# Kernel optimization log

Measured on AMD Instinct MI355X. Metric: run time of the kernel, lower is better.

The kernel has to match this reference:

```python
import jax, jax.numpy as jnp
import numpy as np

N = 100000   # nodes
E = 1600000  # edges (avg degree 16)
G = 512      # graphs in batch
IN = 96      # in_channels
H = 128      # hidden_channels
C = 100      # num_classes
ED = 8       # edge_dim
L = 4        # num_layers
EPS_LN = 1e-5


def setup_inputs() -> dict:
    key = jax.random.key(0)
    ks = jax.random.split(key, 24)
    s = 0.05
    d = {
        "x": jax.random.normal(ks[0], (N, IN), jnp.float32),
        "edge_index": jax.random.randint(ks[1], (2, E), 0, N, jnp.int32),
        "batch": jnp.sort(jax.random.randint(ks[2], (N,), 0, G, jnp.int32)),
        "edge_attr": jax.random.normal(ks[3], (E, ED), jnp.float32),
        # edge encoder MLP: Linear(ED,H) -> ReLU -> Linear(H,1)
        "ee_W1": jax.random.normal(ks[4], (ED, H), jnp.float32) * s,
        "ee_b1": jnp.zeros((H,), jnp.float32),
        "ee_W2": jax.random.normal(ks[5], (H, 1), jnp.float32) * s,
        "ee_b2": jnp.zeros((1,), jnp.float32),
        # GCNConv weights (PyG: lin without bias, bias added after aggregation)
        "W0": jax.random.normal(ks[6], (IN, H), jnp.float32) * s,
        "cb0": jnp.zeros((H,), jnp.float32),
        "W1": jax.random.normal(ks[7], (H, H), jnp.float32) * s,
        "cb1": jnp.zeros((H,), jnp.float32),
        "W2": jax.random.normal(ks[8], (H, H), jnp.float32) * s,
        "cb2": jnp.zeros((H,), jnp.float32),
        "W3": jax.random.normal(ks[9], (H, H), jnp.float32) * s,
        "cb3": jnp.zeros((H,), jnp.float32),
        # LayerNorm params
        "g0": jnp.ones((H,), jnp.float32), "be0": jnp.zeros((H,), jnp.float32),
        "g1": jnp.ones((H,), jnp.float32), "be1": jnp.zeros((H,), jnp.float32),
        "g2": jnp.ones((H,), jnp.float32), "be2": jnp.zeros((H,), jnp.float32),
        "g3": jnp.ones((H,), jnp.float32), "be3": jnp.zeros((H,), jnp.float32),
        # residual projection for layer 0 only (IN != H)
        "res_W": jax.random.normal(ks[10], (IN, H), jnp.float32) * s,
        "res_b": jnp.zeros((H,), jnp.float32),
        # head: Linear(2H,H) -> ReLU -> Linear(H,C)
        "hW1": jax.random.normal(ks[11], (2 * H, H), jnp.float32) * s,
        "hb1": jnp.zeros((H,), jnp.float32),
        "hW2": jax.random.normal(ks[12], (H, C), jnp.float32) * s,
        "hb2": jnp.zeros((C,), jnp.float32),
    }
    return d


def _layer_norm(h, g, b):
    mu = jnp.mean(h, axis=-1, keepdims=True)
    var = jnp.mean(jnp.square(h - mu), axis=-1, keepdims=True)
    return g * (h - mu) / jnp.sqrt(var + EPS_LN) + b


def reference(x, edge_index, batch, edge_attr,
              ee_W1, ee_b1, ee_W2, ee_b2,
              W0, cb0, W1, cb1, W2, cb2, W3, cb3,
              g0, be0, g1, be1, g2, be2, g3, be3,
              res_W, res_b, hW1, hb1, hW2, hb2):
    row, col = edge_index[0], edge_index[1]

    # edge weight = softplus(MLP(edge_attr)) + 1e-4  -> [E]
    eh = jax.nn.relu(edge_attr @ ee_W1 + ee_b1)
    ew = jax.nn.softplus((eh @ ee_W2 + ee_b2)[:, 0]) + 1e-4

    # add self loops with weight 1 (PyG GCNConv default)
    loops = jnp.arange(N, dtype=row.dtype)
    row_sl = jnp.concatenate([row, loops])
    col_sl = jnp.concatenate([col, loops])
    ew_sl = jnp.concatenate([ew, jnp.ones((N,), ew.dtype)])

    # symmetric normalization: D^-1/2 A D^-1/2 (deg over target index)
    deg = jax.ops.segment_sum(ew_sl, col_sl, num_segments=N)
    dis = jnp.where(deg > 0, jax.lax.rsqrt(deg), 0.0)
    norm = dis[row_sl] * ew_sl * dis[col_sl]  # [E+N]

    def conv(h, W, b):
        hw = h @ W                                   # [N,H]
        msg = hw[row_sl] * norm[:, None]             # [E+N,H]
        return jax.ops.segment_sum(msg, col_sl, num_segments=N) + b

    Ws = [W0, W1, W2, W3]
    cbs = [cb0, cb1, cb2, cb3]
    gs = [g0, g1, g2, g3]
    bes = [be0, be1, be2, be3]

    hidden = []
    cur = x
    for i in range(L):
        h = conv(cur, Ws[i], cbs[i])
        h = _layer_norm(h, gs[i], bes[i])
        res = cur @ res_W + res_b if i == 0 else cur
        h = jax.nn.relu(h + res)
        # dropout: eval mode -> identity
        hidden.append(h)
        cur = h
    xm = jnp.mean(jnp.stack(hidden, axis=0), axis=0)  # [N,H]

    # meanmax pooling over graphs
    counts = jax.ops.segment_sum(jnp.ones((N,), xm.dtype), batch, num_segments=G)
    gmean = jax.ops.segment_sum(xm, batch, num_segments=G) / jnp.maximum(counts, 1.0)[:, None]
    gmax = jax.ops.segment_max(xm, batch, num_segments=G)
    gmax = jnp.where(jnp.isfinite(gmax), gmax, 0.0)
    g = jnp.concatenate([gmean, gmax], axis=-1)       # [G,2H]

    # head (dropout identity in eval)
    return jax.nn.relu(g @ hW1 + hb1) @ hW2 + hb2     # [G,C]
```

## Files before the change

kernel.cpp:

```cpp
#include <hip/hip_runtime.h>
#include <hip/hip_fp16.h>
#include <math.h>

#define NN 100000
#define EE 1600000
#define GB 512
#define INC 96
#define HH 128
#define CC 100
#define MAXD 64

typedef __bf16 bf16x8 __attribute__((ext_vector_type(8)));
typedef _Float16 f16x8 __attribute__((ext_vector_type(8)));
typedef float f32x4 __attribute__((ext_vector_type(4)));

__device__ __forceinline__ float unpack_w_f32(unsigned v) {
    return __half2float(__ushort_as_half((unsigned short)(v & 0x7FFFu)));
}
__device__ __forceinline__ __half2 unpack_w_h2(unsigned v) {
    __half h = __ushort_as_half((unsigned short)(v & 0x7FFFu));
    return __halves2half2(h, h);
}

__global__ __launch_bounds__(256) void k_cast(const float* __restrict__ src, __half* __restrict__ dst, int n4) {
    int i = blockIdx.x * 256 + threadIdx.x;
    if (i >= n4) return;
    float4 v = *(const float4*)&src[(size_t)i * 4];
    __half2 a = __floats2half2_rn(v.x, v.y);
    __half2 b = __floats2half2_rn(v.z, v.w);
    *(__half2*)&dst[(size_t)i * 4]     = a;
    *(__half2*)&dst[(size_t)i * 4 + 2] = b;
}

__global__ __launch_bounds__(256) void k_castT(const float* __restrict__ W, __half* __restrict__ Wt, int K) {
    int idx = blockIdx.x * 256 + threadIdx.x;
    if (idx >= K * 128) return;
    int k = idx >> 7, n = idx & 127;
    Wt[(size_t)n * K + k] = __float2half(W[idx]);
}

__global__ __launch_bounds__(512) void k_prep_w1(const float* __restrict__ W1, __bf16* __restrict__ w1f) {
    int tid = threadIdx.x;
    int t = tid >> 6, lane = tid & 63;
    int ln15 = lane & 15, quad = lane >> 4;
    bf16x8 v = {};
    if (quad == 0) {
#pragma unroll
        for (int j = 0; j < 8; ++j) v[j] = (__bf16)W1[j * 128 + t * 16 + ln15];
    }
    *(bf16x8*)&w1f[(size_t)(t * 64 + lane) * 8] = v;
}

__global__ __launch_bounds__(256) void k_edge_mlp_mfma(
    const float* __restrict__ ea,
    const __bf16* __restrict__ w1f, const float* __restrict__ b1,
    const float* __restrict__ W2, const float* __restrict__ b2,
    const int* __restrict__ ei, int* __restrict__ cnt, unsigned* __restrict__ epack)
{
    __shared__ float sDot[128];
    int tid = threadIdx.x, wva = tid >> 6, lane = tid & 63;
    int ln15 = lane & 15, quad = lane >> 4;
    int ebase = blockIdx.x * 128 + wva * 32;

    bf16x8 bfr[8];
#pragma unroll
    for (int t = 0; t < 8; ++t) bfr[t] = *(const bf16x8*)&w1f[(size_t)(t * 64 + lane) * 8];

    bf16x8 a0 = {}, a1 = {};
    if (quad == 0) {
        const float* p0 = &ea[(size_t)(ebase + ln15) * 8];
        float4 u0 = *(const float4*)p0, u1 = *(const float4*)(p0 + 4);
        a0[0] = (__bf16)u0.x; a0[1] = (__bf16)u0.y; a0[2] = (__bf16)u0.z; a0[3] = (__bf16)u0.w;
        a0[4] = (__bf16)u1.x; a0[5] = (__bf16)u1.y; a0[6] = (__bf16)u1.z; a0[7] = (__bf16)u1.w;
        const float* p1 = &ea[(size_t)(ebase + 16 + ln15) * 8];
        float4 w0 = *(const float4*)p1, w1v = *(const float4*)(p1 + 4);
        a1[0] = (__bf16)w0.x; a1[1] = (__bf16)w0.y; a1[2] = (__bf16)w0.z; a1[3] = (__bf16)w0.w;
        a1[4] = (__bf16)w1v.x; a1[5] = (__bf16)w1v.y; a1[6] = (__bf16)w1v.z; a1[7] = (__bf16)w1v.w;
    }

    f32x4 d0 = {0.f, 0.f, 0.f, 0.f}, d1 = {0.f, 0.f, 0.f, 0.f};
#pragma unroll
    for (int t = 0; t < 8; ++t) {
        f32x4 z = {0.f, 0.f, 0.f, 0.f};
        f32x4 c0 = __builtin_amdgcn_mfma_f32_16x16x32_bf16(a0, bfr[t], z, 0, 0, 0);
        f32x4 c1 = __builtin_amdgcn_mfma_f32_16x16x32_bf16(a1, bfr[t], z, 0, 0, 0);
        int col = t * 16 + ln15;
        float b1v = b1[col], w2v = W2[col];
#pragma unroll
        for (int r = 0; r < 4; ++r) {
            float v0 = fmaxf(c0[r] + b1v, 0.0f);
            float v1 = fmaxf(c1[r] + b1v, 0.0f);
            d0[r] = fmaf(v0, w2v, d0[r]);
            d1[r] = fmaf(v1, w2v, d1[r]);
        }
    }
#pragma unroll
    for (int o = 1; o < 16; o <<= 1) {
#pragma unroll
        for (int r = 0; r < 4; ++r) {
            d0[r] += __shfl_xor(d0[r], o, 64);
            d1[r] += __shfl_xor(d1[r], o, 64);
        }
    }
    if (ln15 == 0) {
#pragma unroll
        for (int r = 0; r < 4; ++r) {
            sDot[wva * 32 + quad * 4 + r]      = d0[r];
            sDot[wva * 32 + 16 + quad * 4 + r] = d1[r];
        }
    }
    __syncthreads();
    if (tid < 128) {
        int e = blockIdx.x * 128 + tid;
        float x = sDot[tid] + b2[0];
        float sp = (x > 20.0f) ? x : log1pf(expf(x));
        float wgt = sp + 1e-4f;
        int r = ei[e], c = ei[EE + e];
        int rank = atomicAdd(&cnt[c], 1);
        if (rank < MAXD) {
            unsigned hb = (unsigned)__half_as_ushort(__float2half(wgt)) & 0x7FFFu;
            epack[(size_t)c * MAXD + rank] = ((unsigned)r << 15) | hb;
        }
    }
}

__global__ __launch_bounds__(256) void k_degk(int* __restrict__ cnt, const unsigned* __restrict__ epack,
                                              float* __restrict__ dis, int n) {
    int i = blockIdx.x * 256 + threadIdx.x;
    if (i >= n) return;
    int c = cnt[i]; c = c < MAXD ? c : MAXD;
    cnt[i] = c;
    const unsigned* base = &epack[(size_t)i * MAXD];
    float d = 1.0f;
    for (int k = 0; k < c; ++k) d += unpack_w_f32(base[k]);
    dis[i] = rsqrtf(d);
}

__global__ __launch_bounds__(256) void k_norm(const int* __restrict__ cnt, const float* __restrict__ dis,
                                              unsigned* __restrict__ epack, int n) {
    int wv = threadIdx.x >> 6, lane = threadIdx.x & 63;
    int i = blockIdx.x * 4 + wv;
    if (i >= n) return;
    float dc = dis[i];
    if (lane < cnt[i]) {
        unsigned v = epack[(size_t)i * MAXD + lane];
        float wn = dis[v >> 15] * unpack_w_f32(v) * dc;
        unsigned hb = (unsigned)__half_as_ushort(__float2half(wn)) & 0x7FFFu;
        epack[(size_t)i * MAXD + lane] = (v & 0xFFFF8000u) | hb;
    }
}

__global__ __launch_bounds__(256) void k_gemm_f16(
    const __half* __restrict__ A, const __half* __restrict__ Bt,
    const float* __restrict__ bias, __half* __restrict__ C, int M, int K)
{
    int tid = threadIdx.x;
    int wv = tid >> 6, lane = tid & 63;
    int ln15 = lane & 15, quad = lane >> 4;
    int m0 = blockIdx.x * 64;
    int n0 = wv * 32;
    f32x4 acc[4][2];
#pragma unroll
    for (int mt = 0; mt < 4; ++mt)
#pragma unroll
        for (int nt = 0; nt < 2; ++nt) acc[mt][nt] = (f32x4){0.f, 0.f, 0.f, 0.f};

    int rowm[4];
#pragma unroll
    for (int mt = 0; mt < 4; ++mt) {
        int r = m0 + mt * 16 + ln15;
        rowm[mt] = r < M ? r : M - 1;
    }
    for (int kc = 0; kc < K; kc += 32) {
        f16x8 af[4], bfr[2];
#pragma unroll
        for (int mt = 0; mt < 4; ++mt)
            af[mt] = *(const f16x8*)&A[(size_t)rowm[mt] * K + kc + quad * 8];
#pragma unroll
        for (int nt = 0; nt < 2; ++nt)
            bfr[nt] = *(const f16x8*)&Bt[(size_t)(n0 + nt * 16 + ln15) * K + kc + quad * 8];
#pragma unroll
        for (int mt = 0; mt < 4; ++mt)
#pragma unroll
            for (int nt = 0; nt < 2; ++nt)
                acc[mt][nt] = __builtin_amdgcn_mfma_f32_16x16x32_f16(af[mt], bfr[nt], acc[mt][nt], 0, 0, 0);
    }
#pragma unroll
    for (int nt = 0; nt < 2; ++nt) {
        int col = n0 + nt * 16 + ln15;
        float bv = bias ? bias[col] : 0.0f;
#pragma unroll
        for (int mt = 0; mt < 4; ++mt) {
#pragma unroll
            for (int r = 0; r < 4; ++r) {
                int row = m0 + mt * 16 + quad * 4 + r;
                if (row < M) C[(size_t)row * 128 + col] = __float2half(acc[mt][nt][r] + bv);
            }
        }
    }
}

__global__ __launch_bounds__(256) void k_agg_ln(
    const __half* __restrict__ hw, const float* __restrict__ dis,
    const int* __restrict__ cnt, const unsigned* __restrict__ epack,
    const float* __restrict__ cb, const float* __restrict__ gam,
    const float* __restrict__ bet, const __half* __restrict__ res,
    __half* __restrict__ out, int n)
{
    int wv = threadIdx.x >> 6;
    int lane = threadIdx.x & 63;
    int i = blockIdx.x * 4 + wv;
    if (i >= n) return;
    float di = dis[i];
    float sn = di * di;
    __half2 own = *(const __half2*)&hw[(size_t)i * HH + lane * 2];
    __half hsn = __float2half(sn);
    __half2 acc = __hmul2(own, __halves2half2(hsn, hsn));
    int cn = cnt[i];
    const unsigned* ebase = &epack[(size_t)i * MAXD];
    int k = 0;
    for (; k + 8 <= cn; k += 8) {
        uint4 q0 = *(const uint4*)&ebase[k];
        uint4 q1 = *(const uint4*)&ebase[k + 4];
        __half2 v0 = *(const __half2*)&hw[(size_t)(q0.x >> 15) * HH + lane * 2];
        __half2 v1 = *(const __half2*)&hw[(size_t)(q0.y >> 15) * HH + lane * 2];
        __half2 v2 = *(const __half2*)&hw[(size_t)(q0.z >> 15) * HH + lane * 2];
        __half2 v3 = *(const __half2*)&hw[(size_t)(q0.w >> 15) * HH + lane * 2];
        __half2 v4 = *(const __half2*)&hw[(size_t)(q1.x >> 15) * HH + lane * 2];
        __half2 v5 = *(const __half2*)&hw[(size_t)(q1.y >> 15) * HH + lane * 2];
        __half2 v6 = *(const __half2*)&hw[(size_t)(q1.z >> 15) * HH + lane * 2];
        __half2 v7 = *(const __half2*)&hw[(size_t)(q1.w >> 15) * HH + lane * 2];
        acc = __hfma2(v0, unpack_w_h2(q0.x), acc);
        acc = __hfma2(v1, unpack_w_h2(q0.y), acc);
        acc = __hfma2(v2, unpack_w_h2(q0.z), acc);
        acc = __hfma2(v3, unpack_w_h2(q0.w), acc);
        acc = __hfma2(v4, unpack_w_h2(q1.x), acc);
        acc = __hfma2(v5, unpack_w_h2(q1.y), acc);
        acc = __hfma2(v6, unpack_w_h2(q1.z), acc);
        acc = __hfma2(v7, unpack_w_h2(q1.w), acc);
    }
    for (; k < cn; ++k) {
        unsigned e = ebase[k];
        __half2 v = *(const __half2*)&hw[(size_t)(e >> 15) * HH + lane * 2];
        acc = __hfma2(v, unpack_w_h2(e), acc);
    }
    float2 af = __half22float2(acc);
    float2 cbv = *(const float2*)&cb[lane * 2];
    af.x += cbv.x; af.y += cbv.y;
    float s1 = af.x + af.y;
    float s2 = af.x * af.x + af.y * af.y;
#pragma unroll
    for (int o = 32; o > 0; o >>= 1) {
        s1 += __shfl_xor(s1, o, 64);
        s2 += __shfl_xor(s2, o, 64);
    }
    float mean = s1 * (1.0f / HH);
    float var = fmaxf(s2 * (1.0f / HH) - mean * mean, 0.0f);
    float rstd = rsqrtf(var + 1e-5f);
    float2 gv = *(const float2*)&gam[lane * 2];
    float2 bv = *(const float2*)&bet[lane * 2];
    float2 rv = __half22float2(*(const __half2*)&res[(size_t)i * HH + lane * 2]);
    float hx = fmaxf(fmaf(gv.x, (af.x - mean) * rstd, bv.x) + rv.x, 0.0f);
    float hy = fmaxf(fmaf(gv.y, (af.y - mean) * rstd, bv.y) + rv.y, 0.0f);
    *(__half2*)&out[(size_t)i * HH + lane * 2] = __floats2half2_rn(hx, hy);
}

__global__ __launch_bounds__(128) void k_pool(
    const __half* __restrict__ l0, const __half* __restrict__ l1,
    const __half* __restrict__ l2, const __half* __restrict__ l3,
    const int* __restrict__ batch, float* __restrict__ gbuf, int n)
{
    int g = blockIdx.x, t = threadIdx.x;
    int lo = 0, hi = n;
    while (lo < hi) { int m = (lo + hi) >> 1; if (batch[m] < g) lo = m + 1; else hi = m; }
    int start = lo;
    lo = start; hi = n;
    while (lo < hi) { int m = (lo + hi) >> 1; if (batch[m] < g + 1) lo = m + 1; else hi = m; }
    int end = lo;
    float sum = 0.0f, mx = -INFINITY;
    for (int nd = start; nd < end; ++nd) {
        size_t off = (size_t)nd * HH + t;
        float v = (__half2float(l0[off]) + __half2float(l1[off]) +
                   __half2float(l2[off]) + __half2float(l3[off])) * 0.25f;
        sum += v;
        mx = fmaxf(mx, v);
    }
    int cntg = end - start;
    float mean = sum / fmaxf((float)cntg, 1.0f);
    gbuf[(size_t)g * 256 + t] = mean;
    gbuf[(size_t)g * 256 + 128 + t] = (cntg > 0) ? mx : 0.0f;
}

__global__ __launch_bounds__(128) void k_head(const float* __restrict__ gbuf,
                                              const float* __restrict__ hW1, const float* __restrict__ hb1,
                                              const float* __restrict__ hW2, const float* __restrict__ hb2,
                                              float* __restrict__ out) {
    __shared__ __align__(16) float sg[256];
    __shared__ __align__(16) float sh[128];
    int g = blockIdx.x, t = threadIdx.x;
    sg[t] = gbuf[(size_t)g * 256 + t];
    sg[t + 128] = gbuf[(size_t)g * 256 + 128 + t];
    __syncthreads();
    float h = hb1[t];
    for (int k = 0; k < 256; ++k) h = fmaf(sg[k], hW1[(size_t)k * 128 + t], h);
    sh[t] = fmaxf(h, 0.0f);
    __syncthreads();
    if (t < 100) {
        float o = hb2[t];
        for (int k = 0; k < 128; ++k) o = fmaf(sh[k], hW2[(size_t)k * 100 + t], o);
        out[(size_t)g * 100 + t] = o;
    }
}

extern "C" void kernel_launch(void* const* d_in, const int* in_sizes, int n_in,
                              void* d_out, int out_size, void* d_ws, size_t ws_size,
                              hipStream_t stream) {
    const float* x     = (const float*)d_in[0];
    const int*   ei    = (const int*)d_in[1];
    const int*   batch = (const int*)d_in[2];
    const float* ea    = (const float*)d_in[3];
    const float* eeW1  = (const float*)d_in[4];
    const float* eeb1  = (const float*)d_in[5];
    const float* eeW2  = (const float*)d_in[6];
    const float* eeb2  = (const float*)d_in[7];
    const float* W[4]  = {(const float*)d_in[8], (const float*)d_in[10], (const float*)d_in[12], (const float*)d_in[14]};
    const float* cb[4] = {(const float*)d_in[9], (const float*)d_in[11], (const float*)d_in[13], (const float*)d_in[15]};
    const float* gm[4] = {(const float*)d_in[16], (const float*)d_in[18], (const float*)d_in[20], (const float*)d_in[22]};
    const float* be[4] = {(const float*)d_in[17], (const float*)d_in[19], (const float*)d_in[21], (const float*)d_in[23]};
    const float* resW  = (const float*)d_in[24];
    const float* resb  = (const float*)d_in[25];
    const float* hW1   = (const float*)d_in[26];
    const float* hb1   = (const float*)d_in[27];
    const float* hW2   = (const float*)d_in[28];
    const float* hb2   = (const float*)d_in[29];
    float* out = (float*)d_out;

    char* w = (char*)d_ws;
    auto alloc = [&](size_t bytes) { void* p = w; w += (bytes + 255) & ~(size_t)255; return p; };
    float*    dis    = (float*)   alloc((size_t)NN * 4);
    int*      cnt    = (int*)     alloc((size_t)NN * 4);
    unsigned* epack  = (unsigned*)alloc((size_t)NN * MAXD * 4);
    __half*   xb     = (__half*)  alloc((size_t)NN * INC * 2);
    __half*   hw     = (__half*)  alloc((size_t)NN * HH * 2);
    __half*   lout[4];
    for (int i = 0; i < 4; ++i) lout[i] = (__half*)alloc((size_t)NN * HH * 2);
    float*    gbuf   = (float*)   alloc((size_t)GB * 256 * 4);
    __half*   wt0    = (__half*)  alloc((size_t)INC * HH * 2);
    __half*   wtR    = (__half*)  alloc((size_t)INC * HH * 2);
    __half*   wt1    = (__half*)  alloc((size_t)HH * HH * 2);
    __half*   wt2    = (__half*)  alloc((size_t)HH * HH * 2);
    __half*   wt3    = (__half*)  alloc((size_t)HH * HH * 2);
    __bf16*   w1f    = (__bf16*)  alloc((size_t)8 * 64 * 8 * 2);
    __half*   wtc[4] = {wt0, wt1, wt2, wt3};
    __half*   res0   = lout[1];

    int nblkN = (NN + 255) / 256;
    int nblkEdge = EE / 128;
    int nblkGemm = (NN + 63) / 64;
    int nblkCast = (NN * INC / 4 + 255) / 256;
    int nblkT96 = (INC * 128 + 255) / 256;
    int nblkT128 = (HH * 128 + 255) / 256;

    hipMemsetAsync(cnt, 0, (size_t)NN * 4, stream);
    k_cast<<<nblkCast, 256, 0, stream>>>(x, xb, NN * INC / 4);
    k_castT<<<nblkT96, 256, 0, stream>>>(W[0], wt0, INC);
    k_castT<<<nblkT96, 256, 0, stream>>>(resW, wtR, INC);
    k_castT<<<nblkT128, 256, 0, stream>>>(W[1], wt1, HH);
    k_castT<<<nblkT128, 256, 0, stream>>>(W[2], wt2, HH);
    k_castT<<<nblkT128, 256, 0, stream>>>(W[3], wt3, HH);
    k_prep_w1<<<1, 512, 0, stream>>>(eeW1, w1f);
    k_edge_mlp_mfma<<<nblkEdge, 256, 0, stream>>>(ea, w1f, eeb1, eeW2, eeb2, ei, cnt, epack);
    k_degk<<<nblkN, 256, 0, stream>>>(cnt, epack, dis, NN);
    k_norm<<<(NN + 3) / 4, 256, 0, stream>>>(cnt, dis, epack, NN);

    k_gemm_f16<<<nblkGemm, 256, 0, stream>>>(xb, wt0, nullptr, hw, NN, INC);
    k_gemm_f16<<<nblkGemm, 256, 0, stream>>>(xb, wtR, resb, res0, NN, INC);
    k_agg_ln<<<(NN + 3) / 4, 256, 0, stream>>>(hw, dis, cnt, epack,
                                               cb[0], gm[0], be[0], res0, lout[0], NN);
    for (int l = 1; l < 4; ++l) {
        k_gemm_f16<<<nblkGemm, 256, 0, stream>>>(lout[l - 1], wtc[l], nullptr, hw, NN, HH);
        k_agg_ln<<<(NN + 3) / 4, 256, 0, stream>>>(hw, dis, cnt, epack,
                                                   cb[l], gm[l], be[l], lout[l - 1], lout[l], NN);
    }

    k_pool<<<GB, 128, 0, stream>>>(lout[0], lout[1], lout[2], lout[3], batch, gbuf, NN);
    k_head<<<GB, 128, 0, stream>>>(gbuf, hW1, hb1, hW2, hb2, out);
}
```

Before: 854.3 us.

## Build CSR adjacency via two-pass bucketed scatter instead of global atomics

The edge MLP now only writes per-edge weights. A new split kernel bins edges by destination bucket of 512 nodes using shared-memory histograms and one global atomic per bucket per block. A build kernel then fills each node's packed adjacency list and degree using shared-memory atomics, which replaces the scattered global atomics and the separate degree kernel. The five weight transpose casts are merged into one launch. The cost is an extra edge-weight array and a bucket staging buffer with a fixed capacity per bucket, so edges past that capacity would be silently dropped.

After: 838.0 us. Within noise of the previous version (-1.9%).

```diff
diff --git a/kernel.cpp b/kernel.cpp
--- a/kernel.cpp
+++ b/kernel.cpp
@@ -9,6 +9,10 @@
 #define HH 128
 #define CC 100
 #define MAXD 64
+#define BUCKB 9
+#define NBUK 196
+#define CAPB 10240
+#define EB 4096
 
 typedef __bf16 bf16x8 __attribute__((ext_vector_type(8)));
 typedef _Float16 f16x8 __attribute__((ext_vector_type(8)));
@@ -32,11 +36,23 @@
     *(__half2*)&dst[(size_t)i * 4 + 2] = b;
 }
 
-__global__ __launch_bounds__(256) void k_castT(const float* __restrict__ W, __half* __restrict__ Wt, int K) {
+__global__ __launch_bounds__(256) void k_prep_weights(
+    const float* __restrict__ W0, const float* __restrict__ resW,
+    const float* __restrict__ W1m, const float* __restrict__ W2m, const float* __restrict__ W3m,
+    __half* __restrict__ wt0, __half* __restrict__ wtR,
+    __half* __restrict__ wt1, __half* __restrict__ wt2, __half* __restrict__ wt3)
+{
     int idx = blockIdx.x * 256 + threadIdx.x;
-    if (idx >= K * 128) return;
-    int k = idx >> 7, n = idx & 127;
-    Wt[(size_t)n * K + k] = __float2half(W[idx]);
+    const float* src; __half* dst; int K, base;
+    if (idx < 12288)      { src = W0;   dst = wt0; K = 96;  base = 0; }
+    else if (idx < 24576) { src = resW; dst = wtR; K = 96;  base = 12288; }
+    else if (idx < 40960) { src = W1m;  dst = wt1; K = 128; base = 24576; }
+    else if (idx < 57344) { src = W2m;  dst = wt2; K = 128; base = 40960; }
+    else if (idx < 73728) { src = W3m;  dst = wt3; K = 128; base = 57344; }
+    else return;
+    int l = idx - base;
+    int k = l >> 7, n = l & 127;
+    dst[(size_t)n * K + k] = __float2half(src[l]);
 }
 
 __global__ __launch_bounds__(512) void k_prep_w1(const float* __restrict__ W1, __bf16* __restrict__ w1f) {
@@ -55,7 +71,7 @@
     const float* __restrict__ ea,
     const __bf16* __restrict__ w1f, const float* __restrict__ b1,
     const float* __restrict__ W2, const float* __restrict__ b2,
-    const int* __restrict__ ei, int* __restrict__ cnt, unsigned* __restrict__ epack)
+    float* __restrict__ ew)
 {
     __shared__ float sDot[128];
     int tid = threadIdx.x, wva = tid >> 6, lane = tid & 63;
@@ -114,26 +130,71 @@
         int e = blockIdx.x * 128 + tid;
         float x = sDot[tid] + b2[0];
         float sp = (x > 20.0f) ? x : log1pf(expf(x));
-        float wgt = sp + 1e-4f;
-        int r = ei[e], c = ei[EE + e];
-        int rank = atomicAdd(&cnt[c], 1);
-        if (rank < MAXD) {
-            unsigned hb = (unsigned)__half_as_ushort(__float2half(wgt)) & 0x7FFFu;
-            epack[(size_t)c * MAXD + rank] = ((unsigned)r << 15) | hb;
-        }
-    }
-}
-
-__global__ __launch_bounds__(256) void k_degk(int* __restrict__ cnt, const unsigned* __restrict__ epack,
-                                              float* __restrict__ dis, int n) {
-    int i = blockIdx.x * 256 + threadIdx.x;
-    if (i >= n) return;
-    int c = cnt[i]; c = c < MAXD ? c : MAXD;
-    cnt[i] = c;
-    const unsigned* base = &epack[(size_t)i * MAXD];
-    float d = 1.0f;
-    for (int k = 0; k < c; ++k) d += unpack_w_f32(base[k]);
-    dis[i] = rsqrtf(d);
+        ew[e] = sp + 1e-4f;
+    }
+}
+
+__global__ __launch_bounds__(256) void k_split(const int* __restrict__ ei, const float* __restrict__ ew,
+                                               int* __restrict__ cntB, uint2* __restrict__ barr) {
+    __shared__ unsigned hist[NBUK];
+    __shared__ unsigned gbase[NBUK];
+    __shared__ unsigned short rloc[EB];
+    int tid = threadIdx.x;
+    for (int b = tid; b < NBUK; b += 256) hist[b] = 0;
+    __syncthreads();
+    int e0 = blockIdx.x * EB;
+#pragma unroll
+    for (int j = 0; j < EB / 256; ++j) {
+        int e = e0 + j * 256 + tid;
+        if (e < EE) {
+            int c = ei[EE + e];
+            rloc[j * 256 + tid] = (unsigned short)atomicAdd(&hist[c >> BUCKB], 1u);
+        }
+    }
+    __syncthreads();
+    for (int b = tid; b < NBUK; b += 256)
+        gbase[b] = (hist[b] > 0) ? (unsigned)atomicAdd(&cntB[b], (int)hist[b]) : 0u;
+    __syncthreads();
+#pragma unroll
+    for (int j = 0; j < EB / 256; ++j) {
+        int e = e0 + j * 256 + tid;
+        if (e < EE) {
+            int c = ei[EE + e];
+            int b = c >> BUCKB;
+            unsigned pos = gbase[b] + rloc[j * 256 + tid];
+            if (pos < CAPB) {
+                unsigned hb = (unsigned)__half_as_ushort(__float2half(ew[e])) & 0x7FFFu;
+                barr[(size_t)b * CAPB + pos] = make_uint2(((unsigned)c << 15) | hb, (unsigned)ei[e]);
+            }
+        }
+    }
+}
+
+__global__ __launch_bounds__(256) void k_build(const int* __restrict__ cntB, const uint2* __restrict__ barr,
+                                               unsigned* __restrict__ epack, int* __restrict__ cnt,
+                                               float* __restrict__ dis) {
+    __shared__ unsigned ncnt[512];
+    __shared__ float ndeg[512];
+    int tid = threadIdx.x, b = blockIdx.x;
+    for (int i = tid; i < 512; i += 256) { ncnt[i] = 0; ndeg[i] = 0.0f; }
+    __syncthreads();
+    int n0 = b << BUCKB;
+    int m = cntB[b]; if (m > CAPB) m = CAPB;
+    for (int i = tid; i < m; i += 256) {
+        uint2 rec = barr[(size_t)b * CAPB + i];
+        int c = (int)(rec.x >> 15);
+        int cl = c - n0;
+        unsigned rank = atomicAdd(&ncnt[cl], 1u);
+        if (rank < MAXD) epack[(size_t)c * MAXD + rank] = (rec.y << 15) | (rec.x & 0x7FFFu);
+        atomicAdd(&ndeg[cl], unpack_w_f32(rec.x));
+    }
+    __syncthreads();
+    int nn = NN - n0; if (nn > 512) nn = 512;
+    for (int i = tid; i < nn; i += 256) {
+        unsigned cc = ncnt[i]; if (cc > MAXD) cc = MAXD;
+        cnt[n0 + i] = (int)cc;
+        dis[n0 + i] = rsqrtf(1.0f + ndeg[i]);
+    }
 }
 
 __global__ __launch_bounds__(256) void k_norm(const int* __restrict__ cnt, const float* __restrict__ dis,
@@ -337,8 +398,11 @@
 
     char* w = (char*)d_ws;
     auto alloc = [&](size_t bytes) { void* p = w; w += (bytes + 255) & ~(size_t)255; return p; };
+    float*    ew     = (float*)   alloc((size_t)EE * 4);
     float*    dis    = (float*)   alloc((size_t)NN * 4);
     int*      cnt    = (int*)     alloc((size_t)NN * 4);
+    int*      cntB   = (int*)     alloc((size_t)NBUK * 4);
+    uint2*    barr   = (uint2*)   alloc((size_t)NBUK * CAPB * 8);
     unsigned* epack  = (unsigned*)alloc((size_t)NN * MAXD * 4);
     __half*   xb     = (__half*)  alloc((size_t)NN * INC * 2);
     __half*   hw     = (__half*)  alloc((size_t)NN * HH * 2);
@@ -354,23 +418,18 @@
     __half*   wtc[4] = {wt0, wt1, wt2, wt3};
     __half*   res0   = lout[1];
 
-    int nblkN = (NN + 255) / 256;
     int nblkEdge = EE / 128;
+    int nblkSplit = (EE + EB - 1) / EB;
     int nblkGemm = (NN + 63) / 64;
     int nblkCast = (NN * INC / 4 + 255) / 256;
-    int nblkT96 = (INC * 128 + 255) / 256;
-    int nblkT128 = (HH * 128 + 255) / 256;
-
-    hipMemsetAsync(cnt, 0, (size_t)NN * 4, stream);
+
+    hipMemsetAsync(cntB, 0, (size_t)NBUK * 4, stream);
     k_cast<<<nblkCast, 256, 0, stream>>>(x, xb, NN * INC / 4);
-    k_castT<<<nblkT96, 256, 0, stream>>>(W[0], wt0, INC);
-    k_castT<<<nblkT96, 256, 0, stream>>>(resW, wtR, INC);
-    k_castT<<<nblkT128, 256, 0, stream>>>(W[1], wt1, HH);
-    k_castT<<<nblkT128, 256, 0, stream>>>(W[2], wt2, HH);
-    k_castT<<<nblkT128, 256, 0, stream>>>(W[3], wt3, HH);
+    k_prep_weights<<<288, 256, 0, stream>>>(W[0], resW, W[1], W[2], W[3], wt0, wtR, wt1, wt2, wt3);
     k_prep_w1<<<1, 512, 0, stream>>>(eeW1, w1f);
-    k_edge_mlp_mfma<<<nblkEdge, 256, 0, stream>>>(ea, w1f, eeb1, eeW2, eeb2, ei, cnt, epack);
-    k_degk<<<nblkN, 256, 0, stream>>>(cnt, epack, dis, NN);
+    k_edge_mlp_mfma<<<nblkEdge, 256, 0, stream>>>(ea, w1f, eeb1, eeW2, eeb2, ew);
+    k_split<<<nblkSplit, 256, 0, stream>>>(ei, ew, cntB, barr);
+    k_build<<<NBUK, 256, 0, stream>>>(cntB, barr, epack, cnt, dis);
     k_norm<<<(NN + 3) / 4, 256, 0, stream>>>(cnt, dis, epack, NN);
 
     k_gemm_f16<<<nblkGemm, 256, 0, stream>>>(xb, wt0, nullptr, hw, NN, INC);
```
